# Kernel tuning notes

Measured on AMD Instinct MI355X. Metric: run time of the kernel, lower is better.

Reference implementation:

```python
import jax, jax.numpy as jnp
import numpy as np

DIM = 64
HEADS = 4
WIN = 4


def setup_inputs() -> dict:
    key = jax.random.key(0)
    ks = jax.random.split(key, 9)
    B, C, D, H, W = 2, DIM, 64, 64, 64
    x = jax.random.normal(ks[0], (B, C, D, H, W), dtype=jnp.float32)
    # 1x1x1 Conv3d == pointwise linear: weight [C_out, C_in], bias [C_out]
    def mk(kw, kb):
        return (jax.random.normal(kw, (C, C), dtype=jnp.float32) * 0.05,
                jax.random.normal(kb, (C,), dtype=jnp.float32) * 0.05)
    Wq, bq = mk(ks[1], ks[2])
    Wk, bk = mk(ks[3], ks[4])
    Wv, bv = mk(ks[5], ks[6])
    Wp, bp = mk(ks[7], ks[8])
    return {"x": x, "Wq": Wq, "bq": bq, "Wk": Wk, "bk": bk,
            "Wv": Wv, "bv": bv, "Wp": Wp, "bp": bp}


def reference(x, Wq, bq, Wk, bk, Wv, bv, Wp, bp):
    B, C, D, H, W = x.shape
    w = WIN
    heads = HEADS
    hd = C // heads
    L = w * w * w  # tokens per window (64)
    nd, nh, nw = D // w, H // w, W // w  # spatial dims are multiples of w -> no padding branch
    scale = hd ** -0.5

    # window partition: [B,C,D,H,W] -> [B*nd*nh*nw, C, L]
    xw = (x.reshape(B, C, nd, w, nh, w, nw, w)
            .transpose(0, 2, 4, 6, 1, 3, 5, 7)
            .reshape(B * nd * nh * nw, C, L))

    def pointwise(t, Wm, bm):  # 1x1x1 conv on flattened windows
        return jnp.einsum('ncl,oc->nol', t, Wm) + bm[None, :, None]

    q = pointwise(xw, Wq, bq).reshape(-1, heads, hd, L)
    k = pointwise(xw, Wk, bk).reshape(-1, heads, hd, L)
    v = pointwise(xw, Wv, bv).reshape(-1, heads, hd, L)

    # attn[n,h,i,j] = <q[:, :, :, i], k[:, :, :, j]> * scale ; softmax over j
    attn = jax.nn.softmax(jnp.einsum('nhdi,nhdj->nhij', q, k) * scale, axis=-1)
    # out = v @ attn^T  (dropout is identity in eval)
    out = jnp.einsum('nhdj,nhij->nhdi', v, attn)

    out = out.reshape(-1, C, L)
    out = pointwise(out, Wp, bp)

    # reverse window partition: [B*nd*nh*nw, C, L] -> [B,C,D,H,W]
    out = (out.reshape(B, nd, nh, nw, C, w, w, w)
              .transpose(0, 4, 1, 5, 2, 6, 3, 7)
              .reshape(B, C, D, H, W))
    return out
```

## Files before the change

### kernel.cpp

```cpp
#include <hip/hip_runtime.h>

typedef _Float16 f16;
typedef __attribute__((ext_vector_type(4))) _Float16 f16x4;
typedef __attribute__((ext_vector_type(8))) _Float16 f16x8;
typedef __attribute__((ext_vector_type(4))) float f32x4;

#define MFMA32(a,b,c) __builtin_amdgcn_mfma_f32_16x16x32_f16((a),(b),(c),0,0,0)
#define MFMA16(a,b,c) __builtin_amdgcn_mfma_f32_16x16x16f16((a),(b),(c),0,0,0)

__global__ void wprep(const float* __restrict__ Wq, const float* __restrict__ Wk,
                      const float* __restrict__ Wv, const float* __restrict__ Wp,
                      f16* __restrict__ ws)
{
    const int t = threadIdx.x;
    const int lane = t & 63;
    const float* Wm[4] = {Wq, Wk, Wv, Wp};
    #pragma unroll
    for (int j = 0; j < 8; ++j) {
        const int c = (t >> 6) * 8 + j;
        const int m = c >> 3, ob = (c >> 1) & 3, s = c & 1;
        const float* src = Wm[m] + (ob * 16 + (lane & 15)) * 64 + 8 * (lane >> 4) + 32 * s;
        f32x4 a4 = *(const f32x4*)src;
        f32x4 b4 = *(const f32x4*)(src + 4);
        f16x8 h;
        #pragma unroll
        for (int ii = 0; ii < 8; ++ii) h[ii] = (f16)(ii < 4 ? a4[ii] : b4[ii - 4]);
        *(f16x8*)(ws + c * 512 + lane * 8) = h;
    }
}

__global__ __launch_bounds__(256, 4)
void wsa3d(const float* __restrict__ x, const f16* __restrict__ wsf,
           const float* __restrict__ bq, const float* __restrict__ bk,
           const float* __restrict__ bv, const float* __restrict__ bp,
           float* __restrict__ out)
{
    __shared__ __align__(16) f16 lds[16384];
    f16*   const XW = lds;
    float* const SG = (float*)lds;

    const int tid  = threadIdx.x;
    const int lane = tid & 63;
    const int w    = tid >> 6;
    const int g    = lane >> 4;
    const int ln16 = lane & 15;
    const int key  = ln16 & 7;

    const int bid = blockIdx.x;
    const int Q   = ((bid & 7) << 8) | (bid >> 3);
    const int qx = Q & 3, ih = (Q >> 2) & 15, idz = (Q >> 6) & 15, b = Q >> 10;

    const float c_sc = 0.25f * 1.44269504088896340736f;
    const f32x4 z4 = {0.f, 0.f, 0.f, 0.f};

    const int gz = (lane >> 4) & 3, gy = (lane >> 2) & 3, gq = lane & 3;

    f16x4 valh[16];
    #pragma unroll
    for (int i = 0; i < 16; ++i) {
        const int c = w * 16 + i;
        f32x4 v4 = *(const f32x4*)(x + ((((b*64 + c)*64 + idz*4 + gz)*64) + ih*4 + gy)*64 + qx*16 + gq*4);
        #pragma unroll
        for (int r = 0; r < 4; ++r) valh[i][r] = (f16)v4[r];
    }

    #pragma unroll
    for (int lx = 0; lx < 4; ++lx) {
        const int t = gz * 16 + gy * 4 + lx;
        #pragma unroll
        for (int h2 = 0; h2 < 2; ++h2) {
            f16x8 pk;
            #pragma unroll
            for (int ii = 0; ii < 8; ++ii) pk[ii] = valh[h2 * 8 + ii][lx];
            *(f16x8*)(XW + gq*4096 + t*64 + (((w*2 + h2) ^ (t & 7) ^ gq) << 3)) = pk;
        }
    }
    __syncthreads();

    f16x8 xf[4][2];
    #pragma unroll
    for (int lb = 0; lb < 4; ++lb)
        #pragma unroll
        for (int s = 0; s < 2; ++s)
            xf[lb][s] = *(const f16x8*)(XW + w*4096 + (lb*16 + ln16)*64 + (((g + 4*s) ^ key ^ w) << 3));

    #pragma unroll
    for (int ob = 0; ob < 4; ++ob) {
        f16x8 VF[2];
        #pragma unroll
        for (int s = 0; s < 2; ++s) VF[s] = *(const f16x8*)(wsf + (16 + ob*2 + s)*512 + lane*8);
        const float bvo = bv[ob * 16 + ln16];
        #pragma unroll
        for (int tb = 0; tb < 4; ++tb) {
            f32x4 a = z4;
            #pragma unroll
            for (int s = 0; s < 2; ++s) a = MFMA32(xf[tb][s], VF[s], a);
            f16x4 h4;
            #pragma unroll
            for (int r = 0; r < 4; ++r) h4[r] = (f16)(a[r] + bvo);
            *(f16x4*)(XW + w*4096 + (ob*16 + ln16)*64 + (((2*tb + (g >> 1)) ^ key ^ w) << 3) + 4*(g & 1)) = h4;
        }
    }

    #pragma unroll
    for (int h = 0; h < 4; ++h) {
        f16x8 QF[2], KF[2];
        #pragma unroll
        for (int s = 0; s < 2; ++s) {
            QF[s] = *(const f16x8*)(wsf + (h*2 + s)*512 + lane*8);
            KF[s] = *(const f16x8*)(wsf + (8 + h*2 + s)*512 + lane*8);
        }
        const f32x4 bqv = *(const f32x4*)(bq + h*16 + g*4);
        const f32x4 bkv = *(const f32x4*)(bk + h*16 + g*4);
        f16x4 qf[4], kf[4];
        #pragma unroll
        for (int lb = 0; lb < 4; ++lb) {
            f32x4 aq = z4, ak = z4;
            #pragma unroll
            for (int s = 0; s < 2; ++s) {
                aq = MFMA32(QF[s], xf[lb][s], aq);
                ak = MFMA32(KF[s], xf[lb][s], ak);
            }
            #pragma unroll
            for (int r = 0; r < 4; ++r) {
                qf[lb][r] = (f16)((aq[r] + bqv[r]) * c_sc);
                kf[lb][r] = (f16)(ak[r] + bkv[r]);
            }
        }
        f16x4 va[4];
        #pragma unroll
        for (int jb = 0; jb < 4; ++jb)
            va[jb] = *(const f16x4*)(XW + w*4096 + (16*h + ln16)*64 + (((2*jb + (g >> 1)) ^ key ^ w) << 3) + 4*(g & 1));
        #pragma unroll
        for (int ib = 0; ib < 4; ++ib) {
            f16x4 pf[4];
            f32x4 s4 = z4;
            #pragma unroll
            for (int jb = 0; jb < 4; ++jb) {
                f32x4 S = MFMA16(kf[jb], qf[ib], z4);
                #pragma unroll
                for (int r = 0; r < 4; ++r) {
                    float ev = __builtin_amdgcn_exp2f(S[r]);
                    pf[jb][r] = (f16)ev;
                    s4[r] += ev;
                }
            }
            float hh = (s4[0] + s4[1]) + (s4[2] + s4[3]);
            hh += __shfl_xor(hh, 16);
            hh += __shfl_xor(hh, 32);
            const float inv = __builtin_amdgcn_rcpf(hh);
            f32x4 O = z4;
            #pragma unroll
            for (int jb = 0; jb < 4; ++jb) O = MFMA16(va[jb], pf[jb], O);
            #pragma unroll
            for (int r = 0; r < 4; ++r) {
                const int row = 16*h + 4*g + r;
                XW[w*4096 + row*64 + ((16*ib + ln16) ^ ((4*g + r) << 1))] = (f16)(O[r] * inv);
            }
        }
    }

    f16x8 PFr[4][2];
    #pragma unroll
    for (int oc = 0; oc < 4; ++oc)
        #pragma unroll
        for (int s = 0; s < 2; ++s) PFr[oc][s] = *(const f16x8*)(wsf + (24 + oc*2 + s)*512 + lane*8);
    f32x4 bpv[4];
    #pragma unroll
    for (int oc = 0; oc < 4; ++oc) bpv[oc] = *(const f32x4*)(bp + oc*16 + 4*g);

    f32x4 res[4][4];
    #pragma unroll
    for (int tb = 0; tb < 4; ++tb) {
        f16x8 bf[2];
        #pragma unroll
        for (int s = 0; s < 2; ++s)
            #pragma unroll
            for (int ii = 0; ii < 8; ++ii) {
                const int c = 8*g + 32*s + ii;
                bf[s][ii] = XW[w*4096 + c*64 + ((16*tb + ln16) ^ (((8*g + ii) & 15) << 1))];
            }
        #pragma unroll
        for (int oc = 0; oc < 4; ++oc) {
            f32x4 a = z4;
            a = MFMA32(PFr[oc][0], bf[0], a);
            a = MFMA32(PFr[oc][1], bf[1], a);
            #pragma unroll
            for (int r = 0; r < 4; ++r) res[tb][oc][r] = a[r] + bpv[oc][r];
        }
    }
    __syncthreads();

    #pragma unroll
    for (int oc = 0; oc < 4; ++oc) {
        #pragma unroll
        for (int tb = 0; tb < 4; ++tb)
            #pragma unroll
            for (int r = 0; r < 4; ++r)
                SG[w*1092 + (4*g + r)*68 + ((16*tb + ln16) ^ (w << 2))] = res[tb][oc][r];
        __syncthreads();
        #pragma unroll
        for (int si = 0; si < 4; ++si) {
            const int o2 = w * 4 + si;
            f32x4 v4 = *(const f32x4*)(SG + gq*1092 + o2*68 + ((gz*16 + gy*4) ^ (gq << 2)));
            *(f32x4*)(out + ((((b*64 + oc*16 + o2)*64 + idz*4 + gz)*64) + ih*4 + gy)*64 + qx*16 + gq*4) = v4;
        }
        if (oc < 3) __syncthreads();
    }
}

extern "C" void kernel_launch(void* const* d_in, const int* in_sizes, int n_in,
                              void* d_out, int out_size, void* d_ws, size_t ws_size,
                              hipStream_t stream) {
    (void)in_sizes; (void)n_in; (void)out_size; (void)ws_size;
    const float* x  = (const float*)d_in[0];
    const float* Wq = (const float*)d_in[1];
    const float* bq = (const float*)d_in[2];
    const float* Wk = (const float*)d_in[3];
    const float* bk = (const float*)d_in[4];
    const float* Wv = (const float*)d_in[5];
    const float* bv = (const float*)d_in[6];
    const float* Wp = (const float*)d_in[7];
    const float* bp = (const float*)d_in[8];
    f16* wsf = (f16*)d_ws;
    wprep<<<1, 256, 0, stream>>>(Wq, Wk, Wv, Wp, wsf);
    wsa3d<<<2048, 256, 0, stream>>>(x, wsf, bq, bk, bv, bp, (float*)d_out);
}
```

Measured before the change: 72.59 us.

## Keep attention output in registers and feed projection MFMA directly, store output without LDS

The attention output tiles are kept in registers as fp16 fragments and used directly as MFMA operands for the output projection. This removes the LDS write, the scalar LDS gathers and the LDS staging, along with the barriers used before the global stores. A second, differently packed copy of Wp is prepared in the workspace to match the new operand layout. Each lane now writes float4 chunks straight to global memory, which costs more register pressure and possibly less coalesced stores.

```diff
diff --git a/kernel.cpp b/kernel.cpp
--- a/kernel.cpp
+++ b/kernel.cpp
@@ -27,6 +27,16 @@
         for (int ii = 0; ii < 8; ++ii) h[ii] = (f16)(ii < 4 ? a4[ii] : b4[ii - 4]);
         *(f16x8*)(ws + c * 512 + lane * 8) = h;
     }
+    #pragma unroll
+    for (int j = 0; j < 4; ++j) {
+        const int f = (t >> 6) * 4 + j;
+        const int oc = f >> 2, hh = f & 3;
+        f32x4 wv = *(const f32x4*)(Wp + (oc * 16 + (lane & 15)) * 64 + 16 * hh + 4 * (lane >> 4));
+        f16x4 h4;
+        #pragma unroll
+        for (int r = 0; r < 4; ++r) h4[r] = (f16)wv[r];
+        *(f16x4*)(ws + 16384 + f * 256 + lane * 4) = h4;
+    }
 }
 
 __global__ __launch_bounds__(256, 4)
@@ -35,9 +45,7 @@
            const float* __restrict__ bv, const float* __restrict__ bp,
            float* __restrict__ out)
 {
-    __shared__ __align__(16) f16 lds[16384];
-    f16*   const XW = lds;
-    float* const SG = (float*)lds;
+    __shared__ __align__(16) f16 XW[16384];
 
     const int tid  = threadIdx.x;
     const int lane = tid & 63;
@@ -102,6 +110,7 @@
         }
     }
 
+    f16x4 ot[4][4];
     #pragma unroll
     for (int h = 0; h < 4; ++h) {
         f16x8 QF[2], KF[2];
@@ -153,59 +162,27 @@
             #pragma unroll
             for (int jb = 0; jb < 4; ++jb) O = MFMA16(va[jb], pf[jb], O);
             #pragma unroll
-            for (int r = 0; r < 4; ++r) {
-                const int row = 16*h + 4*g + r;
-                XW[w*4096 + row*64 + ((16*ib + ln16) ^ ((4*g + r) << 1))] = (f16)(O[r] * inv);
-            }
-        }
-    }
-
-    f16x8 PFr[4][2];
-    #pragma unroll
-    for (int oc = 0; oc < 4; ++oc)
-        #pragma unroll
-        for (int s = 0; s < 2; ++s) PFr[oc][s] = *(const f16x8*)(wsf + (24 + oc*2 + s)*512 + lane*8);
-    f32x4 bpv[4];
-    #pragma unroll
-    for (int oc = 0; oc < 4; ++oc) bpv[oc] = *(const f32x4*)(bp + oc*16 + 4*g);
-
-    f32x4 res[4][4];
-    #pragma unroll
-    for (int tb = 0; tb < 4; ++tb) {
-        f16x8 bf[2];
-        #pragma unroll
-        for (int s = 0; s < 2; ++s)
-            #pragma unroll
-            for (int ii = 0; ii < 8; ++ii) {
-                const int c = 8*g + 32*s + ii;
-                bf[s][ii] = XW[w*4096 + c*64 + ((16*tb + ln16) ^ (((8*g + ii) & 15) << 1))];
-            }
-        #pragma unroll
-        for (int oc = 0; oc < 4; ++oc) {
+            for (int r = 0; r < 4; ++r) ot[h][ib][r] = (f16)(O[r] * inv);
+        }
+    }
+
+    const f16* ws2 = wsf + 16384;
+    #pragma unroll
+    for (int oc = 0; oc < 4; ++oc) {
+        const float bpo = bp[oc * 16 + ln16];
+        f16x4 wb[4];
+        #pragma unroll
+        for (int h = 0; h < 4; ++h)
+            wb[h] = *(const f16x4*)(ws2 + (oc * 4 + h) * 256 + lane * 4);
+        #pragma unroll
+        for (int ib = 0; ib < 4; ++ib) {
             f32x4 a = z4;
-            a = MFMA32(PFr[oc][0], bf[0], a);
-            a = MFMA32(PFr[oc][1], bf[1], a);
-            #pragma unroll
-            for (int r = 0; r < 4; ++r) res[tb][oc][r] = a[r] + bpv[oc][r];
-        }
-    }
-    __syncthreads();
-
-    #pragma unroll
-    for (int oc = 0; oc < 4; ++oc) {
-        #pragma unroll
-        for (int tb = 0; tb < 4; ++tb)
-            #pragma unroll
-            for (int r = 0; r < 4; ++r)
-                SG[w*1092 + (4*g + r)*68 + ((16*tb + ln16) ^ (w << 2))] = res[tb][oc][r];
-        __syncthreads();
-        #pragma unroll
-        for (int si = 0; si < 4; ++si) {
-            const int o2 = w * 4 + si;
-            f32x4 v4 = *(const f32x4*)(SG + gq*1092 + o2*68 + ((gz*16 + gy*4) ^ (gq << 2)));
-            *(f32x4*)(out + ((((b*64 + oc*16 + o2)*64 + idz*4 + gz)*64) + ih*4 + gy)*64 + qx*16 + gq*4) = v4;
-        }
-        if (oc < 3) __syncthreads();
+            #pragma unroll
+            for (int h = 0; h < 4; ++h) a = MFMA16(ot[h][ib], wb[h], a);
+            #pragma unroll
+            for (int r = 0; r < 4; ++r) a[r] += bpo;
+            *(f32x4*)(out + ((((b*64 + oc*16 + ln16)*64 + idz*4 + ib)*64) + ih*4 + g)*64 + qx*16 + w*4) = a;
+        }
     }
 }
 
```

New measurement: 84.07 us. 15.8% more time.
